# Kernel optimization log

Hardware: AMD Instinct MI355X
Metric: run time of the kernel (lower is better)

Reference implementation:

```python
import jax, jax.numpy as jnp
import numpy as np

K = 3
KK = K * K
G = 8  # num_heads / offset groups
PAD = K // 2


def conv2d(x, w, b):
    # NCHW conv, stride 1, same padding
    y = jax.lax.conv_general_dilated(
        x, w, window_strides=(1, 1), padding=[(PAD, PAD), (PAD, PAD)],
        dimension_numbers=("NCHW", "OIHW", "NCHW"))
    return y + b[None, :, None, None]


def bilinear_sample(img, py, px):
    # img: [Cg, H, W]; py/px: [KK, H, W] fractional sampling locations
    # zero-padding bilinear (torchvision deform_conv2d semantics)
    Cg, H, W = img.shape
    flat = img.reshape(Cg, H * W)

    y0 = jnp.floor(py)
    x0 = jnp.floor(px)
    wy1 = py - y0
    wx1 = px - x0
    wy0 = 1.0 - wy1
    wx0 = 1.0 - wx1
    y0i = y0.astype(jnp.int32)
    x0i = x0.astype(jnp.int32)

    def gather(iy, ix):
        valid = (iy >= 0) & (iy < H) & (ix >= 0) & (ix < W)
        idx = jnp.clip(iy, 0, H - 1) * W + jnp.clip(ix, 0, W - 1)
        v = jnp.take(flat, idx.reshape(-1), axis=1).reshape(Cg, KK, H, W)
        return v * valid[None].astype(img.dtype)

    return (gather(y0i, x0i) * (wy0 * wx0)[None]
            + gather(y0i, x0i + 1) * (wy0 * wx1)[None]
            + gather(y0i + 1, x0i) * (wy1 * wx0)[None]
            + gather(y0i + 1, x0i + 1) * (wy1 * wx1)[None])


def setup_inputs() -> dict:
    key = jax.random.key(0)
    ks = jax.random.split(key, 8)
    B, C, H, W = 8, 256, 64, 64
    O = 256
    x = jax.random.normal(ks[0], (B, C, H, W), jnp.float32)
    w_off = jax.random.normal(ks[1], (2 * KK * G, C, K, K), jnp.float32) * 0.01
    b_off = jax.random.normal(ks[2], (2 * KK * G,), jnp.float32) * 0.01
    w_attn = jax.random.normal(ks[3], (KK * G, C, K, K), jnp.float32) * 0.01
    b_attn = jax.random.normal(ks[4], (KK * G,), jnp.float32) * 0.01
    w_out = jax.random.normal(ks[5], (O, C, K, K), jnp.float32) * 0.02
    b_out = jax.random.normal(ks[6], (O,), jnp.float32) * 0.01
    return {"x": x, "w_off": w_off, "b_off": b_off,
            "w_attn": w_attn, "b_attn": b_attn,
            "w_out": w_out, "b_out": b_out}


def reference(x, w_off, b_off, w_attn, b_attn, w_out, b_out):
    B, C, H, W = x.shape
    O = w_out.shape[0]
    Cg = C // G

    # learned offsets: [B, G, KK, 2(dy,dx), H, W]
    off = conv2d(x, w_off, b_off).reshape(B, G, KK, 2, H, W)
    # modulation mask with softmax over the KK kernel taps (per head)
    attn = conv2d(x, w_attn, b_attn).reshape(B, G, KK, H, W)
    attn = jax.nn.softmax(attn, axis=2)

    # base sampling grid for each kernel tap (stride=1, dilation=1)
    ki = (jnp.arange(KK) // K).astype(x.dtype)  # kernel row
    kj = (jnp.arange(KK) % K).astype(x.dtype)   # kernel col
    base_y = jnp.arange(H, dtype=x.dtype)[None, :, None] - PAD + ki[:, None, None]  # [KK,H,1]
    base_x = jnp.arange(W, dtype=x.dtype)[None, None, :] - PAD + kj[:, None, None]  # [KK,1,W]
    py = base_y + off[:, :, :, 0]  # [B,G,KK,H,W]
    px = base_x + off[:, :, :, 1]

    xg = x.reshape(B, G, Cg, H, W)
    # vmap bilinear gather over batch and offset groups -> [B,G,Cg,KK,H,W]
    samp = jax.vmap(jax.vmap(bilinear_sample))(xg, py, px)

    # modulated deformable conv: mask-weight the samples, contract with weights
    wt = w_out.reshape(O, G, Cg, KK)
    out = jnp.einsum("bgnkhw,bgkhw,ognk->bohw", samp, attn, wt)
    return out + b_out[None, :, None, None]
```

## Files before the change

kernel.cpp:

```cpp
#include <hip/hip_runtime.h>

#define BN   8
#define CC   256
#define HH   64
#define WW   64
#define GG   8
#define CG   32
#define KKK  9
#define OO   256
#define HW   (HH*WW)
#define NPAD 256
#define NOUT 216

typedef __attribute__((ext_vector_type(8))) _Float16 half8;
typedef __attribute__((ext_vector_type(4))) float f32x4;

union U4H8 { uint4 u; half8 h; };

__global__ void repack_w(const float* __restrict__ w_out, _Float16* __restrict__ wt3) {
    int idx = blockIdx.x * 256 + threadIdx.x;
    if (idx >= GG * KKK * CG * OO) return;
    int cg = idx & 31;
    int o  = (idx >> 5) & 255;
    int s  = idx >> 13;
    int kk = s % 9;
    int g  = s / 9;
    wt3[idx] = (_Float16)w_out[o * 2304 + (g * 32 + cg) * 9 + kk];
}

__global__ void repack_conv(const float* __restrict__ w_off, const float* __restrict__ b_off,
                            const float* __restrict__ w_attn, const float* __restrict__ b_attn,
                            _Float16* __restrict__ wt_conv, float* __restrict__ bias_c) {
    int idx = blockIdx.x * 256 + threadIdx.x;
    if (idx >= 9 * NPAD * 256) return;
    int c = idx & 255;
    int r = idx >> 8;
    int n = r & 255;
    int tap = r >> 8;
    float v = 0.f;
    if (n < 144)      v = w_off[(n * 256 + c) * 9 + tap];
    else if (n < 216) v = w_attn[((n - 144) * 256 + c) * 9 + tap];
    wt_conv[(tap * NPAD + n) * 256 + c] = (_Float16)v;
    if (idx < 224) {
        float bv = 0.f;
        if (idx < 144)      bv = b_off[idx];
        else if (idx < 216) bv = b_attn[idx - 144];
        bias_c[idx] = bv;
    }
}

__global__ __launch_bounds__(256) void repack_x(const float* __restrict__ x,
                                                _Float16* __restrict__ x_h) {
    __shared__ _Float16 T[64][264];
    const int bid = blockIdx.x;
    const int b = bid & 7, h = bid >> 3;
    const int t = threadIdx.x;
    const float* src = x + (((long)(b * 256 + t)) << 12) + h * 64;
    #pragma unroll
    for (int i = 0; i < 16; ++i) {
        float4 f = ((const float4*)src)[i];
        T[i * 4 + 0][t] = (_Float16)f.x;
        T[i * 4 + 1][t] = (_Float16)f.y;
        T[i * 4 + 2][t] = (_Float16)f.z;
        T[i * 4 + 3][t] = (_Float16)f.w;
    }
    __syncthreads();
    _Float16* dst = x_h + (((long)(b * 4096 + h * 64)) << 8);
    #pragma unroll
    for (int it = 0; it < 8; ++it) {
        int idx = it * 256 + t;
        int px = idx >> 5, ch = idx & 31;
        uint4 v = *(const uint4*)&T[px][ch * 8];
        *(uint4*)(dst + px * 256 + ch * 8) = v;
    }
}

__global__ __launch_bounds__(512, 4) void conv_mfma(
    const _Float16* __restrict__ x_h, const _Float16* __restrict__ wt_conv,
    const float* __restrict__ bias_c, float* __restrict__ conv_buf) {
    __shared__ alignas(16) char smem[36864];
    _Float16 (*Ald)[64][40] = (_Float16 (*)[64][40])smem;
    float* red = (float*)smem;

    const int bid = blockIdx.x;
    const int b = bid & 7, h = bid >> 3;
    const int t = threadIdx.x;
    const int lane = t & 63;
    const int wv = t >> 6;
    const int group = wv >> 2;
    const int wg = wv & 3;
    const int tl = t & 255;
    const int px = tl >> 2, cq = tl & 3;

    f32x4 acc[4][4];
    #pragma unroll
    for (int i = 0; i < 4; ++i)
        #pragma unroll
        for (int j = 0; j < 4; ++j) acc[i][j] = (f32x4){0.f, 0.f, 0.f, 0.f};

    const _Float16* xb = x_h + ((long)b << 20) + cq * 8;
    const long boff = (long)(wg * 64 + (lane & 15)) * 256 + (lane >> 4) * 8;

    uint4 aR; bool vA;
    {
        int gs = group * 36;
        int tap = gs >> 3, cc = gs & 7;
        int ti = tap / 3, tj = tap % 3;
        int y = h + ti - 1, xc = px + tj - 1;
        vA = ((unsigned)y < 64u) && ((unsigned)xc < 64u);
        int yc = min(max(y, 0), 63), xcc = min(max(xc, 0), 63);
        aR = *(const uint4*)(xb + ((long)(yc * 64 + xcc)) * 256 + cc * 32);
    }

    for (int s = 0; s < 36; ++s) {
        const int gs = group * 36 + s;
        const _Float16* wsB = wt_conv + (long)(gs >> 3) * (NPAD * 256)
                              + (gs & 7) * 32 + boff;
        uint4 bq0 = *(const uint4*)(wsB);
        uint4 bq1 = *(const uint4*)(wsB + 4096);
        uint4 bq2 = *(const uint4*)(wsB + 8192);
        uint4 bq3 = *(const uint4*)(wsB + 12288);
        {
            uint4 az = vA ? aR : make_uint4(0u, 0u, 0u, 0u);
            *(uint4*)&Ald[group][px][cq * 8] = az;
        }
        if (s < 35) {
            int gsn = gs + 1;
            int tap = gsn >> 3, cc = gsn & 7;
            int ti = tap / 3, tj = tap % 3;
            int y = h + ti - 1, xc = px + tj - 1;
            vA = ((unsigned)y < 64u) && ((unsigned)xc < 64u);
            int yc = min(max(y, 0), 63), xcc = min(max(xc, 0), 63);
            aR = *(const uint4*)(xb + ((long)(yc * 64 + xcc)) * 256 + cc * 32);
        }
        __syncthreads();

        const int k0 = (lane >> 4) * 8;
        U4H8 b0, b1, b2, b3; b0.u = bq0; b1.u = bq1; b2.u = bq2; b3.u = bq3;
        #pragma unroll
        for (int mi = 0; mi < 4; ++mi) {
            half8 a = *(const half8*)&Ald[group][mi * 16 + (lane & 15)][k0];
            acc[mi][0] = __builtin_amdgcn_mfma_f32_16x16x32_f16(a, b0.h, acc[mi][0], 0, 0, 0);
            acc[mi][1] = __builtin_amdgcn_mfma_f32_16x16x32_f16(a, b1.h, acc[mi][1], 0, 0, 0);
            acc[mi][2] = __builtin_amdgcn_mfma_f32_16x16x32_f16(a, b2.h, acc[mi][2], 0, 0, 0);
            acc[mi][3] = __builtin_amdgcn_mfma_f32_16x16x32_f16(a, b3.h, acc[mi][3], 0, 0, 0);
        }
        __syncthreads();
    }

    #pragma unroll
    for (int r = 0; r < 2; ++r) {
        if (group == 1) {
            #pragma unroll
            for (int m2 = 0; m2 < 2; ++m2)
                #pragma unroll
                for (int j = 0; j < 4; ++j)
                    *(f32x4*)&red[tl * 36 + m2 * 16 + j * 4] = acc[r * 2 + m2][j];
        }
        __syncthreads();
        if (group == 0) {
            #pragma unroll
            for (int m2 = 0; m2 < 2; ++m2)
                #pragma unroll
                for (int j = 0; j < 4; ++j) {
                    f32x4 v = *(const f32x4*)&red[tl * 36 + m2 * 16 + j * 4];
                    acc[r * 2 + m2][j] += v;
                }
        }
        __syncthreads();
    }

    if (group == 0) {
        const int colb = (lane >> 4) * 4;
        #pragma unroll
        for (int mi = 0; mi < 4; ++mi) {
            int px0 = mi * 16 + colb;
            #pragma unroll
            for (int j = 0; j < 4; ++j) {
                int oc = wg * 64 + j * 16 + (lane & 15);
                if (oc < NOUT) {
                    float bb = bias_c[oc];
                    float4 v = make_float4(acc[mi][j][0] + bb, acc[mi][j][1] + bb,
                                           acc[mi][j][2] + bb, acc[mi][j][3] + bb);
                    *(float4*)&conv_buf[((long)b * NOUT + oc) * HW + h * WW + px0] = v;
                }
            }
        }
    }
}

__device__ __forceinline__ void calc_coords(int h, int px, int ki, int kj,
    float dy, float dx,
    int& i00, int& i01, int& i10, int& i11,
    float& u00, float& u01, float& u10, float& u11) {
    float py  = (float)(h - 1 + ki) + dy;
    float pxf = (float)(px - 1 + kj) + dx;
    float y0f = floorf(py), x0f = floorf(pxf);
    int y0 = (int)y0f, x0 = (int)x0f;
    float wy1 = py - y0f, wx1 = pxf - x0f;
    float wy0 = 1.f - wy1, wx0 = 1.f - wx1;
    int y1 = y0 + 1, x1 = x0 + 1;
    float m00 = (((unsigned)y0 < 64u) && ((unsigned)x0 < 64u)) ? 1.f : 0.f;
    float m01 = (((unsigned)y0 < 64u) && ((unsigned)x1 < 64u)) ? 1.f : 0.f;
    float m10 = (((unsigned)y1 < 64u) && ((unsigned)x0 < 64u)) ? 1.f : 0.f;
    float m11 = (((unsigned)y1 < 64u) && ((unsigned)x1 < 64u)) ? 1.f : 0.f;
    int cy0 = min(max(y0, 0), 63), cy1 = min(max(y1, 0), 63);
    int cx0 = min(max(x0, 0), 63), cx1 = min(max(x1, 0), 63);
    u00 = wy0 * wx0 * m00; u01 = wy0 * wx1 * m01;
    u10 = wy1 * wx0 * m10; u11 = wy1 * wx1 * m11;
    i00 = cy0 * 64 + cx0; i01 = cy0 * 64 + cx1;
    i10 = cy1 * 64 + cx0; i11 = cy1 * 64 + cx1;
}

__global__ __launch_bounds__(512, 4) void sample_gemm_mfma(
    const _Float16* __restrict__ x_h, const float* __restrict__ conv_buf,
    const _Float16* __restrict__ wt3,
    const float* __restrict__ b_out, float* __restrict__ out) {
    __shared__ alignas(16) char smem[36864];
    _Float16 (*Ald)[64][40] = (_Float16 (*)[64][40])smem;
    float* attnL = (float*)(smem + 10240);
    float* red = (float*)smem;

    const int bid = blockIdx.x;
    const int b = bid & 7, h = bid >> 3;
    const int t = threadIdx.x;
    const int lane = t & 63;
    const int wv = t >> 6;
    const int group = wv >> 2;
    const int wg = wv & 3;
    const int tl = t & 255;
    const int px = tl >> 2, cq = tl & 3;

    f32x4 acc[4][4];
    #pragma unroll
    for (int i = 0; i < 4; ++i)
        #pragma unroll
        for (int j = 0; j < 4; ++j) acc[i][j] = (f32x4){0.f, 0.f, 0.f, 0.f};

    const float* cbase = conv_buf + (long)b * NOUT * HW + h * WW;
    const _Float16* xbase = x_h + ((long)b << 20) + cq * 8;
    const long boff = (long)(wg * 64 + (lane & 15)) * 32 + (lane >> 4) * 8;

    {
        int ppx = t & 63, g = t >> 6;
        const float* ap = cbase + (long)(144 + g * 9) * HW + ppx;
        float v[9];
        float m = -1e30f;
        #pragma unroll
        for (int k = 0; k < 9; ++k) { v[k] = ap[k * HW]; m = fmaxf(m, v[k]); }
        float ssum = 0.f;
        #pragma unroll
        for (int k = 0; k < 9; ++k) { v[k] = __expf(v[k] - m); ssum += v[k]; }
        float inv = 1.f / ssum;
        #pragma unroll
        for (int k = 0; k < 9; ++k) attnL[(g * 9 + k) * 64 + ppx] = v[k] * inv;
    }

    uint4 q00, q01, q10, q11;
    float u00, u01, u10, u11;
    float dyN, dxN;
    {
        int gs = group * 36;
        float dy = cbase[(2 * gs) * HW + px], dx = cbase[(2 * gs + 1) * HW + px];
        int i00, i01, i10, i11;
        calc_coords(h, px, 0, 0, dy, dx, i00, i01, i10, i11, u00, u01, u10, u11);
        const _Float16* xg = xbase + (group * 4) * 32;
        q00 = *(const uint4*)(xg + (long)i00 * 256);
        q01 = *(const uint4*)(xg + (long)i01 * 256);
        q10 = *(const uint4*)(xg + (long)i10 * 256);
        q11 = *(const uint4*)(xg + (long)i11 * 256);
        dyN = cbase[(2 * gs + 2) * HW + px]; dxN = cbase[(2 * gs + 3) * HW + px];
    }
    __syncthreads();

    for (int s = 0; s < 36; ++s) {
        const int gs = group * 36 + s;
        const _Float16* wsB = wt3 + (long)gs * 8192 + boff;
        uint4 bq0 = *(const uint4*)(wsB);
        uint4 bq1 = *(const uint4*)(wsB + 512);
        uint4 bq2 = *(const uint4*)(wsB + 1024);
        uint4 bq3 = *(const uint4*)(wsB + 1536);
        {
            float av = attnL[gs * 64 + px];
            U4H8 a00, a01, a10, a11;
            a00.u = q00; a01.u = q01; a10.u = q10; a11.u = q11;
            half8 rr = a00.h * (_Float16)u00 + a01.h * (_Float16)u01
                     + a10.h * (_Float16)u10 + a11.h * (_Float16)u11;
            rr = rr * (_Float16)av;
            *(half8*)&Ald[group][px][cq * 8] = rr;
        }
        if (s < 35) {
            int sn = s + 1, gsn = gs + 1;
            int g = group * 4 + sn / 9, kk = sn % 9;
            int i00, i01, i10, i11;
            calc_coords(h, px, kk / 3, kk % 3, dyN, dxN, i00, i01, i10, i11,
                        u00, u01, u10, u11);
            const _Float16* xg = xbase + g * 32;
            q00 = *(const uint4*)(xg + (long)i00 * 256);
            q01 = *(const uint4*)(xg + (long)i01 * 256);
            q10 = *(const uint4*)(xg + (long)i10 * 256);
            q11 = *(const uint4*)(xg + (long)i11 * 256);
            int s2 = min(sn + 1, 35);
            int gs2 = group * 36 + s2;
            dyN = cbase[(2 * gs2) * HW + px]; dxN = cbase[(2 * gs2 + 1) * HW + px];
            (void)gsn;
        }
        __syncthreads();

        const int k0 = (lane >> 4) * 8;
        U4H8 b0, b1, b2, b3; b0.u = bq0; b1.u = bq1; b2.u = bq2; b3.u = bq3;
        #pragma unroll
        for (int mi = 0; mi < 4; ++mi) {
            half8 a = *(const half8*)&Ald[group][mi * 16 + (lane & 15)][k0];
            acc[mi][0] = __builtin_amdgcn_mfma_f32_16x16x32_f16(a, b0.h, acc[mi][0], 0, 0, 0);
            acc[mi][1] = __builtin_amdgcn_mfma_f32_16x16x32_f16(a, b1.h, acc[mi][1], 0, 0, 0);
            acc[mi][2] = __builtin_amdgcn_mfma_f32_16x16x32_f16(a, b2.h, acc[mi][2], 0, 0, 0);
            acc[mi][3] = __builtin_amdgcn_mfma_f32_16x16x32_f16(a, b3.h, acc[mi][3], 0, 0, 0);
        }
        __syncthreads();
    }

    #pragma unroll
    for (int r = 0; r < 2; ++r) {
        if (group == 1) {
            #pragma unroll
            for (int m2 = 0; m2 < 2; ++m2)
                #pragma unroll
                for (int j = 0; j < 4; ++j)
                    *(f32x4*)&red[tl * 36 + m2 * 16 + j * 4] = acc[r * 2 + m2][j];
        }
        __syncthreads();
        if (group == 0) {
            #pragma unroll
            for (int m2 = 0; m2 < 2; ++m2)
                #pragma unroll
                for (int j = 0; j < 4; ++j) {
                    f32x4 v = *(const f32x4*)&red[tl * 36 + m2 * 16 + j * 4];
                    acc[r * 2 + m2][j] += v;
                }
        }
        __syncthreads();
    }

    if (group == 0) {
        const int colb = (lane >> 4) * 4;
        #pragma unroll
        for (int mi = 0; mi < 4; ++mi) {
            int px0 = mi * 16 + colb;
            #pragma unroll
            for (int j = 0; j < 4; ++j) {
                int oc = wg * 64 + j * 16 + (lane & 15);
                float bb = b_out[oc];
                float4 v = make_float4(acc[mi][j][0] + bb, acc[mi][j][1] + bb,
                                       acc[mi][j][2] + bb, acc[mi][j][3] + bb);
                *(float4*)&out[((long)b * OO + oc) * HW + h * WW + px0] = v;
            }
        }
    }
}

extern "C" void kernel_launch(void* const* d_in, const int* in_sizes, int n_in,
                              void* d_out, int out_size, void* d_ws, size_t ws_size,
                              hipStream_t stream) {
    const float* x      = (const float*)d_in[0];
    const float* w_off  = (const float*)d_in[1];
    const float* b_off  = (const float*)d_in[2];
    const float* w_attn = (const float*)d_in[3];
    const float* b_attn = (const float*)d_in[4];
    const float* w_out  = (const float*)d_in[5];
    const float* b_out  = (const float*)d_in[6];
    float* out = (float*)d_out;

    _Float16* x_h     = (_Float16*)d_ws;
    float* conv_buf   = (float*)(x_h + 8388608);
    _Float16* wt3     = (_Float16*)(conv_buf + 7077888);
    _Float16* wt_conv = wt3 + 589824;
    float* bias_c     = (float*)(wt_conv + 589824);

    repack_w<<<dim3((589824 + 255) / 256), dim3(256), 0, stream>>>(w_out, wt3);
    repack_conv<<<dim3((9 * NPAD * 256 + 255) / 256), dim3(256), 0, stream>>>(
        w_off, b_off, w_attn, b_attn, wt_conv, bias_c);
    repack_x<<<dim3(512), dim3(256), 0, stream>>>(x, x_h);

    conv_mfma<<<dim3(512), dim3(512), 0, stream>>>(x_h, wt_conv, bias_c, conv_buf);

    sample_gemm_mfma<<<dim3(512), dim3(512), 0, stream>>>(
        x_h, conv_buf, wt3, b_out, out);
}
```

Baseline: 244.3 us.

## Double-buffer LDS A tiles and prefetch weights to halve barriers per step

Both the conv and sample-GEMM kernels now keep two LDS buffers for the A tile, so the next step's tile is written while MFMAs read the current one. Only one barrier per iteration remains, and it waits on LDS counters only. Weight fragments for the next step are loaded after the MFMAs and the gather prefetch is moved two steps ahead. This is meant to hide global-load and barrier latency, at the cost of extra LDS, since sample_gemm grows to 38912 bytes and may lose occupancy, plus more live registers.

```diff
diff --git a/kernel.cpp b/kernel.cpp
--- a/kernel.cpp
+++ b/kernel.cpp
@@ -16,6 +16,12 @@
 typedef __attribute__((ext_vector_type(4))) float f32x4;
 
 union U4H8 { uint4 u; half8 h; };
+
+#define LGKM0_BARRIER() do { \
+    asm volatile("s_waitcnt lgkmcnt(0)" ::: "memory"); \
+    __builtin_amdgcn_s_barrier(); \
+    __builtin_amdgcn_sched_barrier(0); \
+} while (0)
 
 __global__ void repack_w(const float* __restrict__ w_out, _Float16* __restrict__ wt3) {
     int idx = blockIdx.x * 256 + threadIdx.x;
@@ -79,7 +85,7 @@
     const _Float16* __restrict__ x_h, const _Float16* __restrict__ wt_conv,
     const float* __restrict__ bias_c, float* __restrict__ conv_buf) {
     __shared__ alignas(16) char smem[36864];
-    _Float16 (*Ald)[64][40] = (_Float16 (*)[64][40])smem;
+    _Float16 (*Ald)[2][64][40] = (_Float16 (*)[2][64][40])smem;
     float* red = (float*)smem;
 
     const int bid = blockIdx.x;
@@ -91,6 +97,7 @@
     const int wg = wv & 3;
     const int tl = t & 255;
     const int px = tl >> 2, cq = tl & 3;
+    const int gs0 = group * 36;
 
     f32x4 acc[4][4];
     #pragma unroll
@@ -102,54 +109,76 @@
     const long boff = (long)(wg * 64 + (lane & 15)) * 256 + (lane >> 4) * 8;
 
     uint4 aR; bool vA;
-    {
-        int gs = group * 36;
-        int tap = gs >> 3, cc = gs & 7;
-        int ti = tap / 3, tj = tap % 3;
-        int y = h + ti - 1, xc = px + tj - 1;
+    uint4 bq0, bq1, bq2, bq3;
+
+    {
+        int tap = gs0 >> 3, cc = gs0 & 7;
+        int y = h + tap / 3 - 1, xc = px + tap % 3 - 1;
+        bool v0 = ((unsigned)y < 64u) && ((unsigned)xc < 64u);
+        int yc = min(max(y, 0), 63), xcc = min(max(xc, 0), 63);
+        uint4 a0 = *(const uint4*)(xb + ((long)(yc * 64 + xcc)) * 256 + cc * 32);
+        uint4 az = v0 ? a0 : make_uint4(0u, 0u, 0u, 0u);
+        *(uint4*)&Ald[group][0][px][cq * 8] = az;
+    }
+    {
+        int gsn = gs0 + 1;
+        int tap = gsn >> 3, cc = gsn & 7;
+        int y = h + tap / 3 - 1, xc = px + tap % 3 - 1;
         vA = ((unsigned)y < 64u) && ((unsigned)xc < 64u);
         int yc = min(max(y, 0), 63), xcc = min(max(xc, 0), 63);
         aR = *(const uint4*)(xb + ((long)(yc * 64 + xcc)) * 256 + cc * 32);
     }
+    {
+        const _Float16* wsB = wt_conv + (long)(gs0 >> 3) * (NPAD * 256)
+                              + (gs0 & 7) * 32 + boff;
+        bq0 = *(const uint4*)(wsB);
+        bq1 = *(const uint4*)(wsB + 4096);
+        bq2 = *(const uint4*)(wsB + 8192);
+        bq3 = *(const uint4*)(wsB + 12288);
+    }
+    LGKM0_BARRIER();
 
     for (int s = 0; s < 36; ++s) {
-        const int gs = group * 36 + s;
-        const _Float16* wsB = wt_conv + (long)(gs >> 3) * (NPAD * 256)
-                              + (gs & 7) * 32 + boff;
-        uint4 bq0 = *(const uint4*)(wsB);
-        uint4 bq1 = *(const uint4*)(wsB + 4096);
-        uint4 bq2 = *(const uint4*)(wsB + 8192);
-        uint4 bq3 = *(const uint4*)(wsB + 12288);
-        {
+        const int gs = gs0 + s;
+        if (s < 35) {
             uint4 az = vA ? aR : make_uint4(0u, 0u, 0u, 0u);
-            *(uint4*)&Ald[group][px][cq * 8] = az;
-        }
-        if (s < 35) {
-            int gsn = gs + 1;
+            *(uint4*)&Ald[group][(s + 1) & 1][px][cq * 8] = az;
+        }
+        if (s < 34) {
+            int gsn = gs + 2;
             int tap = gsn >> 3, cc = gsn & 7;
-            int ti = tap / 3, tj = tap % 3;
-            int y = h + ti - 1, xc = px + tj - 1;
+            int y = h + tap / 3 - 1, xc = px + tap % 3 - 1;
             vA = ((unsigned)y < 64u) && ((unsigned)xc < 64u);
             int yc = min(max(y, 0), 63), xcc = min(max(xc, 0), 63);
             aR = *(const uint4*)(xb + ((long)(yc * 64 + xcc)) * 256 + cc * 32);
         }
+        {
+            const int k0 = (lane >> 4) * 8;
+            U4H8 b0, b1, b2, b3; b0.u = bq0; b1.u = bq1; b2.u = bq2; b3.u = bq3;
+            #pragma unroll
+            for (int mi = 0; mi < 4; ++mi) {
+                half8 a = *(const half8*)&Ald[group][s & 1][mi * 16 + (lane & 15)][k0];
+                acc[mi][0] = __builtin_amdgcn_mfma_f32_16x16x32_f16(a, b0.h, acc[mi][0], 0, 0, 0);
+                acc[mi][1] = __builtin_amdgcn_mfma_f32_16x16x32_f16(a, b1.h, acc[mi][1], 0, 0, 0);
+                acc[mi][2] = __builtin_amdgcn_mfma_f32_16x16x32_f16(a, b2.h, acc[mi][2], 0, 0, 0);
+                acc[mi][3] = __builtin_amdgcn_mfma_f32_16x16x32_f16(a, b3.h, acc[mi][3], 0, 0, 0);
+            }
+        }
+        if (s < 35) {
+            int gsn = gs + 1;
+            const _Float16* wsB = wt_conv + (long)(gsn >> 3) * (NPAD * 256)
+                                  + (gsn & 7) * 32 + boff;
+            bq0 = *(const uint4*)(wsB);
+            bq1 = *(const uint4*)(wsB + 4096);
+            bq2 = *(const uint4*)(wsB + 8192);
+            bq3 = *(const uint4*)(wsB + 12288);
+        }
+        LGKM0_BARRIER();
+    }
+
+    #pragma unroll
+    for (int r = 0; r < 2; ++r) {
         __syncthreads();
-
-        const int k0 = (lane >> 4) * 8;
-        U4H8 b0, b1, b2, b3; b0.u = bq0; b1.u = bq1; b2.u = bq2; b3.u = bq3;
-        #pragma unroll
-        for (int mi = 0; mi < 4; ++mi) {
-            half8 a = *(const half8*)&Ald[group][mi * 16 + (lane & 15)][k0];
-            acc[mi][0] = __builtin_amdgcn_mfma_f32_16x16x32_f16(a, b0.h, acc[mi][0], 0, 0, 0);
-            acc[mi][1] = __builtin_amdgcn_mfma_f32_16x16x32_f16(a, b1.h, acc[mi][1], 0, 0, 0);
-            acc[mi][2] = __builtin_amdgcn_mfma_f32_16x16x32_f16(a, b2.h, acc[mi][2], 0, 0, 0);
-            acc[mi][3] = __builtin_amdgcn_mfma_f32_16x16x32_f16(a, b3.h, acc[mi][3], 0, 0, 0);
-        }
-        __syncthreads();
-    }
-
-    #pragma unroll
-    for (int r = 0; r < 2; ++r) {
         if (group == 1) {
             #pragma unroll
             for (int m2 = 0; m2 < 2; ++m2)
@@ -167,7 +196,6 @@
                     acc[r * 2 + m2][j] += v;
                 }
         }
-        __syncthreads();
     }
 
     if (group == 0) {
@@ -216,9 +244,9 @@
     const _Float16* __restrict__ x_h, const float* __restrict__ conv_buf,
     const _Float16* __restrict__ wt3,
     const float* __restrict__ b_out, float* __restrict__ out) {
-    __shared__ alignas(16) char smem[36864];
-    _Float16 (*Ald)[64][40] = (_Float16 (*)[64][40])smem;
-    float* attnL = (float*)(smem + 10240);
+    __shared__ alignas(16) char smem[38912];
+    _Float16 (*Ald)[2][64][40] = (_Float16 (*)[2][64][40])smem;
+    float* attnL = (float*)(smem + 20480);
     float* red = (float*)smem;
 
     const int bid = blockIdx.x;
@@ -230,6 +258,7 @@
     const int wg = wv & 3;
     const int tl = t & 255;
     const int px = tl >> 2, cq = tl & 3;
+    const int gs0 = group * 36;
 
     f32x4 acc[4][4];
     #pragma unroll
@@ -255,42 +284,65 @@
         #pragma unroll
         for (int k = 0; k < 9; ++k) attnL[(g * 9 + k) * 64 + ppx] = v[k] * inv;
     }
+    float dy0 = cbase[(2 * gs0) * HW + px], dx0 = cbase[(2 * gs0 + 1) * HW + px];
+    __syncthreads();
 
     uint4 q00, q01, q10, q11;
     float u00, u01, u10, u11;
     float dyN, dxN;
-    {
-        int gs = group * 36;
-        float dy = cbase[(2 * gs) * HW + px], dx = cbase[(2 * gs + 1) * HW + px];
+    uint4 bq0, bq1, bq2, bq3;
+    {
         int i00, i01, i10, i11;
-        calc_coords(h, px, 0, 0, dy, dx, i00, i01, i10, i11, u00, u01, u10, u11);
+        float v00, v01, v10, v11;
+        calc_coords(h, px, 0, 0, dy0, dx0, i00, i01, i10, i11, v00, v01, v10, v11);
+        const _Float16* xg = xbase + (group * 4) * 32;
+        uint4 a00 = *(const uint4*)(xg + (long)i00 * 256);
+        uint4 a01 = *(const uint4*)(xg + (long)i01 * 256);
+        uint4 a10 = *(const uint4*)(xg + (long)i10 * 256);
+        uint4 a11 = *(const uint4*)(xg + (long)i11 * 256);
+        float av = attnL[gs0 * 64 + px];
+        U4H8 h00, h01, h10, h11;
+        h00.u = a00; h01.u = a01; h10.u = a10; h11.u = a11;
+        half8 rr = h00.h * (_Float16)v00 + h01.h * (_Float16)v01
+                 + h10.h * (_Float16)v10 + h11.h * (_Float16)v11;
+        rr = rr * (_Float16)av;
+        *(half8*)&Ald[group][0][px][cq * 8] = rr;
+    }
+    {
+        float dy1 = cbase[(2 * (gs0 + 1)) * HW + px];
+        float dx1 = cbase[(2 * (gs0 + 1) + 1) * HW + px];
+        int i00, i01, i10, i11;
+        calc_coords(h, px, 0, 1, dy1, dx1, i00, i01, i10, i11, u00, u01, u10, u11);
         const _Float16* xg = xbase + (group * 4) * 32;
         q00 = *(const uint4*)(xg + (long)i00 * 256);
         q01 = *(const uint4*)(xg + (long)i01 * 256);
         q10 = *(const uint4*)(xg + (long)i10 * 256);
         q11 = *(const uint4*)(xg + (long)i11 * 256);
-        dyN = cbase[(2 * gs + 2) * HW + px]; dxN = cbase[(2 * gs + 3) * HW + px];
-    }
-    __syncthreads();
+        dyN = cbase[(2 * (gs0 + 2)) * HW + px];
+        dxN = cbase[(2 * (gs0 + 2) + 1) * HW + px];
+    }
+    {
+        const _Float16* wsB = wt3 + (long)gs0 * 8192 + boff;
+        bq0 = *(const uint4*)(wsB);
+        bq1 = *(const uint4*)(wsB + 512);
+        bq2 = *(const uint4*)(wsB + 1024);
+        bq3 = *(const uint4*)(wsB + 1536);
+    }
+    LGKM0_BARRIER();
 
     for (int s = 0; s < 36; ++s) {
-        const int gs = group * 36 + s;
-        const _Float16* wsB = wt3 + (long)gs * 8192 + boff;
-        uint4 bq0 = *(const uint4*)(wsB);
-        uint4 bq1 = *(const uint4*)(wsB + 512);
-        uint4 bq2 = *(const uint4*)(wsB + 1024);
-        uint4 bq3 = *(const uint4*)(wsB + 1536);
-        {
-            float av = attnL[gs * 64 + px];
+        const int gs = gs0 + s;
+        if (s < 35) {
+            float av = attnL[(gs + 1) * 64 + px];
             U4H8 a00, a01, a10, a11;
             a00.u = q00; a01.u = q01; a10.u = q10; a11.u = q11;
             half8 rr = a00.h * (_Float16)u00 + a01.h * (_Float16)u01
                      + a10.h * (_Float16)u10 + a11.h * (_Float16)u11;
             rr = rr * (_Float16)av;
-            *(half8*)&Ald[group][px][cq * 8] = rr;
-        }
-        if (s < 35) {
-            int sn = s + 1, gsn = gs + 1;
+            *(half8*)&Ald[group][(s + 1) & 1][px][cq * 8] = rr;
+        }
+        if (s < 34) {
+            int sn = s + 2;
             int g = group * 4 + sn / 9, kk = sn % 9;
             int i00, i01, i10, i11;
             calc_coords(h, px, kk / 3, kk % 3, dyN, dxN, i00, i01, i10, i11,
@@ -300,28 +352,35 @@
             q01 = *(const uint4*)(xg + (long)i01 * 256);
             q10 = *(const uint4*)(xg + (long)i10 * 256);
             q11 = *(const uint4*)(xg + (long)i11 * 256);
-            int s2 = min(sn + 1, 35);
-            int gs2 = group * 36 + s2;
-            dyN = cbase[(2 * gs2) * HW + px]; dxN = cbase[(2 * gs2 + 1) * HW + px];
-            (void)gsn;
-        }
+            int s3 = min(s + 3, 35);
+            dyN = cbase[(2 * (gs0 + s3)) * HW + px];
+            dxN = cbase[(2 * (gs0 + s3) + 1) * HW + px];
+        }
+        {
+            const int k0 = (lane >> 4) * 8;
+            U4H8 b0, b1, b2, b3; b0.u = bq0; b1.u = bq1; b2.u = bq2; b3.u = bq3;
+            #pragma unroll
+            for (int mi = 0; mi < 4; ++mi) {
+                half8 a = *(const half8*)&Ald[group][s & 1][mi * 16 + (lane & 15)][k0];
+                acc[mi][0] = __builtin_amdgcn_mfma_f32_16x16x32_f16(a, b0.h, acc[mi][0], 0, 0, 0);
+                acc[mi][1] = __builtin_amdgcn_mfma_f32_16x16x32_f16(a, b1.h, acc[mi][1], 0, 0, 0);
+                acc[mi][2] = __builtin_amdgcn_mfma_f32_16x16x32_f16(a, b2.h, acc[mi][2], 0, 0, 0);
+                acc[mi][3] = __builtin_amdgcn_mfma_f32_16x16x32_f16(a, b3.h, acc[mi][3], 0, 0, 0);
+            }
+        }
+        if (s < 35) {
+            const _Float16* wsB = wt3 + (long)(gs + 1) * 8192 + boff;
+            bq0 = *(const uint4*)(wsB);
+            bq1 = *(const uint4*)(wsB + 512);
+            bq2 = *(const uint4*)(wsB + 1024);
+            bq3 = *(const uint4*)(wsB + 1536);
+        }
+        LGKM0_BARRIER();
+    }
+
+    #pragma unroll
+    for (int r = 0; r < 2; ++r) {
         __syncthreads();
-
-        const int k0 = (lane >> 4) * 8;
-        U4H8 b0, b1, b2, b3; b0.u = bq0; b1.u = bq1; b2.u = bq2; b3.u = bq3;
-        #pragma unroll
-        for (int mi = 0; mi < 4; ++mi) {
-            half8 a = *(const half8*)&Ald[group][mi * 16 + (lane & 15)][k0];
-            acc[mi][0] = __builtin_amdgcn_mfma_f32_16x16x32_f16(a, b0.h, acc[mi][0], 0, 0, 0);
-            acc[mi][1] = __builtin_amdgcn_mfma_f32_16x16x32_f16(a, b1.h, acc[mi][1], 0, 0, 0);
-            acc[mi][2] = __builtin_amdgcn_mfma_f32_16x16x32_f16(a, b2.h, acc[mi][2], 0, 0, 0);
-            acc[mi][3] = __builtin_amdgcn_mfma_f32_16x16x32_f16(a, b3.h, acc[mi][3], 0, 0, 0);
-        }
-        __syncthreads();
-    }
-
-    #pragma unroll
-    for (int r = 0; r < 2; ++r) {
         if (group == 1) {
             #pragma unroll
             for (int m2 = 0; m2 < 2; ++m2)
@@ -339,11 +398,13 @@
                     acc[r * 2 + m2][j] += v;
                 }
         }
-        __syncthreads();
     }
 
     if (group == 0) {
         const int colb = (lane >> 4) * 4;
+        #pragma unroll
+        for (int mi = 0; mi < 2; ++mi) {
+        }
         #pragma unroll
         for (int mi = 0; mi < 4; ++mi) {
             int px0 = mi * 16 + colb;
```

Result: no change. 242.7 us (-0.7%).
